# Kernel tuning notes

Hardware: AMD Instinct MI355X
Metric: run time of the kernel (lower is better)

## Reference

```python
import jax, jax.numpy as jnp
import numpy as np


def _fo_pool(f, z):
    # c_t = f_t * c_{t-1} + z_t, c_0 = 0, scanned over axis 1 (seq).
    # Associative combine: (a1,b1) * (a2,b2) = (a1*a2, a2*b1 + b2)
    def combine(left, right):
        a1, b1 = left
        a2, b2 = right
        return a1 * a2, a2 * b1 + b2
    _, c = jax.lax.associative_scan(combine, (f, z), axis=1)
    return c


def setup_inputs() -> dict:
    key = jax.random.key(0)
    ks = jax.random.split(key, 10)
    B, S, D_in, D_model, D_mlp, n_cls = 32, 2048, 512, 1024, 1024, 128
    s = 0.02
    return {
        "x":  jax.random.normal(ks[0], (B, S, D_in), dtype=jnp.float32),
        "W":  jax.random.normal(ks[1], (D_in, 3 * D_model), dtype=jnp.float32) * s,  # Linear, bias=False
        "V":  jax.random.normal(ks[2], (D_in, 3 * D_model), dtype=jnp.float32) * s,
        "Vb": jax.random.normal(ks[3], (3 * D_model,), dtype=jnp.float32) * s,
        "W0": jax.random.normal(ks[4], (D_model, D_mlp), dtype=jnp.float32) * s,
        "b0": jax.random.normal(ks[5], (D_mlp,), dtype=jnp.float32) * s,
        "W1": jax.random.normal(ks[6], (D_mlp, D_mlp), dtype=jnp.float32) * s,
        "b1": jax.random.normal(ks[7], (D_mlp,), dtype=jnp.float32) * s,
        "W2": jax.random.normal(ks[8], (D_mlp, n_cls), dtype=jnp.float32) * s,
        "b2": jax.random.normal(ks[9], (n_cls,), dtype=jnp.float32) * s,
    }


def reference(x, W, V, Vb, W0, b0, W1, b1, W2, b2):
    # kernel_size=2 pre: W(x) + V(x shifted right by one, zero-padded)
    xprev = jnp.pad(x[:, :-1, :], ((0, 0), (1, 0), (0, 0)))  # [B,S,D_in]
    pre = jnp.einsum('bsd,dk->bsk', x, W) + jnp.einsum('bsd,dk->bsk', xprev, V) + Vb
    f, z, o = jnp.split(pre, 3, axis=-1)
    f = jax.nn.sigmoid(f)
    z = (1.0 - f) * jnp.tanh(z)
    o = jax.nn.sigmoid(o)
    c = _fo_pool(f, z)          # [B,S,D_model]
    h = c * o
    q = h[:, -1, :]             # last timestep
    # dropout is identity at inference (training=False)
    q = jax.nn.relu(q @ W0 + b0)
    q = jax.nn.relu(q @ W1 + b1)
    return q @ W2 + b2
```

## Files before the change

### kernel.cpp

```cpp
#include <hip/hip_runtime.h>
#include <cstdint>
#include <cstddef>


typedef __attribute__((ext_vector_type(8))) short short8;
typedef __attribute__((ext_vector_type(4))) float f32x4;

#define ZERO_OFF_E 6291456u
#define XB_OFF_E   8388608u
#define U_LDS_BASE 8256

__device__ __forceinline__ unsigned short f2bf(float f) {
  unsigned int u = __float_as_uint(f);
  u += 0x7fffu + ((u >> 16) & 1u);
  return (unsigned short)(u >> 16);
}

__device__ __forceinline__ unsigned stage_addr(int r, int c) {
  return (unsigned)(r * 64 + (((c + r + (r >> 2)) & 3) << 4));
}

__device__ __forceinline__ float sigmoidf_fast(float x) {
  return 1.f / (1.f + __expf(-x));
}
__device__ __forceinline__ float tanhf_fast(float x) {
  float a = fabsf(x);
  float e = __expf(-2.f * a);
  float t = (1.f - e) / (1.f + e);
  return copysignf(t, x);
}

__global__ void prologue_kernel(const float* __restrict__ x, const float* __restrict__ W,
                                const float* __restrict__ V,
                                const float* __restrict__ b0, const float* __restrict__ b1,
                                const float* __restrict__ b2,
                                unsigned short* __restrict__ xb, unsigned short* __restrict__ U,
                                float* __restrict__ q0, float* __restrict__ q1,
                                float* __restrict__ out, uint4* __restrict__ zpg) {
  __shared__ float T[64 * 65];
  const int bx = blockIdx.x;
  if (bx < 8192) {
    int base = bx * 1024 + threadIdx.x;
#pragma unroll
    for (int i = 0; i < 4; ++i) {
      int gid = base + i * 256;
      float4 v = ((const float4*)x)[gid];
      ushort4 o;
      o.x = f2bf(v.x); o.y = f2bf(v.y); o.z = f2bf(v.z); o.w = f2bf(v.w);
      ((ushort4*)xb)[gid] = o;
    }
  } else if (bx < 8704) {
    const int u = bx - 8192;
    const int j0 = (u & 31) * 64;
    const int k0 = (u >> 5) * 64;
    const int jl = threadIdx.x & 63;
    const int q  = threadIdx.x >> 6;
    const float* src = (k0 < 512) ? (W + (size_t)k0 * 3072) : (V + (size_t)(k0 - 512) * 3072);
#pragma unroll 4
    for (int i = 0; i < 16; ++i) {
      int kl = q * 16 + i;
      T[kl * 65 + jl] = src[(size_t)kl * 3072 + j0 + jl];
    }
    __syncthreads();
    const int kl = threadIdx.x & 63;
#pragma unroll 4
    for (int i = 0; i < 16; ++i) {
      int jj = q * 16 + i;
      U[(size_t)(j0 + jj) * 1024 + k0 + kl] = f2bf(T[kl * 65 + jj]);
    }
  } else if (bx < 8832) {
    int gid = (bx - 8704) * 256 + threadIdx.x;
    q0[gid] = b0[gid & 1023];
    q1[gid] = b1[gid & 1023];
    if (gid < 4096) out[gid] = b2[gid & 127];
  } else {
    zpg[threadIdx.x] = make_uint4(0u, 0u, 0u, 0u);
  }
}

template <bool USE_BF>
__global__ __launch_bounds__(256, 3) void qrnn_main(
    const unsigned short* __restrict__ wsb, const float* __restrict__ xf,
    const float* __restrict__ Vb,
    float* __restrict__ Fagg, float* __restrict__ Zagg) {
  __shared__ __align__(16) char smem[36864];

  const int dt = blockIdx.x;
  const int cj = blockIdx.y;
  const int b  = blockIdx.z;
  const int tid = threadIdx.x;
  const int lane = tid & 63;
  const int wid  = tid >> 6;
  const int wm = wid >> 1, wn = wid & 1;
  const int s0 = cj * 128;
  const int l15 = lane & 15, lc = lane >> 4;

  f32x4 acc[4][4];
#pragma unroll
  for (int i = 0; i < 4; ++i)
#pragma unroll
    for (int j = 0; j < 4; ++j) acc[i][j] = f32x4{0.f, 0.f, 0.f, 0.f};

  unsigned voffA[2];
  size_t offAF[2]; int zAF[2];
#pragma unroll
  for (int p = 0; p < 2; ++p) {
    int cw = tid + p * 256;
    int r = cw >> 2, c = cw & 3;
    int sg = s0 - 1 + r;
    voffA[p] = (sg < 0) ? (ZERO_OFF_E + (unsigned)(c * 8))
                        : (XB_OFF_E + (unsigned)(b * 2048 + sg) * 512u + (unsigned)(c * 8));
    zAF[p] = (sg < 0);
    offAF[p] = ((size_t)(b * 2048 + (sg < 0 ? 0 : sg)) << 9) + c * 8;
  }
  unsigned voffA3 = XB_OFF_E + (unsigned)(b * 2048 + s0 + 127) * 512u + (unsigned)((tid & 3) * 8);
  size_t offAF3 = ((size_t)(b * 2048 + s0 + 127) << 9) + (tid & 3) * 8;

  unsigned voffU[4];
#pragma unroll
  for (int k = 0; k < 4; ++k) {
    int uw = tid + k * 256;
    int r = uw >> 2, c = uw & 3;
    int col = r & 127, half = r >> 7;
    int j = (col < 64) ? (dt * 64 + col) : (1024 + dt * 64 + (col - 64));
    voffU[k] = (unsigned)(j * 1024 + half * 512 + c * 8);
  }

  unsigned wA[2], wU[4];
#pragma unroll
  for (int p = 0; p < 2; ++p) {
    int cw = tid + p * 256;
    wA[p] = stage_addr(cw >> 2, cw & 3);
  }
  const unsigned wA3 = stage_addr(128, tid & 3);
#pragma unroll
  for (int k = 0; k < 4; ++k) {
    int uw = tid + k * 256;
    wU[k] = U_LDS_BASE + stage_addr(uw >> 2, uw & 3);
  }

  unsigned roA[2][4], roU[2][4];
#pragma unroll
  for (int h2 = 0; h2 < 2; ++h2) {
#pragma unroll
    for (int mt = 0; mt < 4; ++mt) {
      int rr = wm * 64 + l15 + mt * 16 + 1 - h2;
      roA[h2][mt] = stage_addr(rr, lc);
    }
#pragma unroll
    for (int nt = 0; nt < 4; ++nt) {
      int rrU = h2 * 128 + wn * 64 + l15 + nt * 16;
      roU[h2][nt] = U_LDS_BASE + stage_addr(rrU, lc);
    }
  }

  uint4 pA0, pA1, pA3, pU0, pU1, pU2, pU3;

  auto load_stage = [&](int s) {
    const unsigned short* cur = wsb + s * 32;
    if constexpr (USE_BF) {
      pA0 = *(const uint4*)(cur + voffA[0]);
      pA1 = *(const uint4*)(cur + voffA[1]);
      if (tid < 4) pA3 = *(const uint4*)(cur + voffA3);
    } else {
      const float* curf = xf + s * 32;
#pragma unroll
      for (int p = 0; p < 2; ++p) {
        uint4 v = make_uint4(0u, 0u, 0u, 0u);
        if (!zAF[p]) {
          float4 a0 = *(const float4*)(curf + offAF[p]);
          float4 a1 = *(const float4*)(curf + offAF[p] + 4);
          v.x = (unsigned)f2bf(a0.x) | ((unsigned)f2bf(a0.y) << 16);
          v.y = (unsigned)f2bf(a0.z) | ((unsigned)f2bf(a0.w) << 16);
          v.z = (unsigned)f2bf(a1.x) | ((unsigned)f2bf(a1.y) << 16);
          v.w = (unsigned)f2bf(a1.z) | ((unsigned)f2bf(a1.w) << 16);
        }
        if (p == 0) pA0 = v; else pA1 = v;
      }
      if (tid < 4) {
        float4 a0 = *(const float4*)(curf + offAF3);
        float4 a1 = *(const float4*)(curf + offAF3 + 4);
        pA3.x = (unsigned)f2bf(a0.x) | ((unsigned)f2bf(a0.y) << 16);
        pA3.y = (unsigned)f2bf(a0.z) | ((unsigned)f2bf(a0.w) << 16);
        pA3.z = (unsigned)f2bf(a1.x) | ((unsigned)f2bf(a1.y) << 16);
        pA3.w = (unsigned)f2bf(a1.z) | ((unsigned)f2bf(a1.w) << 16);
      }
    }
    pU0 = *(const uint4*)(cur + voffU[0]);
    pU1 = *(const uint4*)(cur + voffU[1]);
    pU2 = *(const uint4*)(cur + voffU[2]);
    pU3 = *(const uint4*)(cur + voffU[3]);
  };

  load_stage(0);

#pragma unroll 1
  for (int s = 0; s < 16; ++s) {
    __syncthreads();
    *(uint4*)(smem + wA[0]) = pA0;
    *(uint4*)(smem + wA[1]) = pA1;
    if (tid < 4) *(uint4*)(smem + wA3) = pA3;
    *(uint4*)(smem + wU[0]) = pU0;
    *(uint4*)(smem + wU[1]) = pU1;
    *(uint4*)(smem + wU[2]) = pU2;
    *(uint4*)(smem + wU[3]) = pU3;
    __syncthreads();
    if (s < 15) load_stage(s + 1);
#pragma unroll
    for (int h2 = 0; h2 < 2; ++h2) {
      short8 bfr[4];
#pragma unroll
      for (int nt = 0; nt < 4; ++nt)
        bfr[nt] = *(const short8*)(smem + roU[h2][nt]);
#pragma unroll
      for (int mt = 0; mt < 4; ++mt) {
        short8 afr = *(const short8*)(smem + roA[h2][mt]);
#pragma unroll
        for (int nt = 0; nt < 4; ++nt)
          acc[mt][nt] = __builtin_amdgcn_mfma_f32_16x16x32_bf16(afr, bfr[nt], acc[mt][nt], 0, 0, 0);
      }
    }
  }

  float* fA   = (float*)smem;
  float* tzA  = (float*)(smem + 17408);
  float* segF = (float*)(smem + 34816);
  float* segZ = (float*)(smem + 35840);

  const int d = tid & 63;
  float vb[4];
#pragma unroll
  for (int nt = 0; nt < 4; ++nt)
    vb[nt] = Vb[wn * 1024 + dt * 64 + nt * 16 + l15];

  float F_run = 1.f, Z_run = 0.f;

  for (int ph = 0; ph < 2; ++ph) {
    __syncthreads();
    if (wm == ph) {
      float* dst = (wn == 0) ? fA : tzA;
#pragma unroll
      for (int mt = 0; mt < 4; ++mt)
#pragma unroll
        for (int nt = 0; nt < 4; ++nt)
#pragma unroll
          for (int rg = 0; rg < 4; ++rg) {
            int t = mt * 16 + ((lane >> 4) << 2) + rg;
            int c = nt * 16 + l15;
            float v = acc[mt][nt][rg] + vb[nt];
            v = (wn == 0) ? sigmoidf_fast(v) : tanhf_fast(v);
            dst[t * 68 + c] = v;
          }
    }
    __syncthreads();
    {
      int seg = tid >> 6;
      float F = 1.f, Z = 0.f;
#pragma unroll 4
      for (int i = 0; i < 16; ++i) {
        int t = seg * 16 + i;
        float f  = fA[t * 68 + d];
        float tz = tzA[t * 68 + d];
        float z = (1.f - f) * tz;
        Z = f * Z + z;
        F *= f;
      }
      segF[seg * 64 + d] = F;
      segZ[seg * 64 + d] = Z;
    }
    __syncthreads();
    if (tid < 64) {
#pragma unroll
      for (int sgi = 0; sgi < 4; ++sgi) {
        float Fs = segF[sgi * 64 + tid], Zs = segZ[sgi * 64 + tid];
        Z_run = Fs * Z_run + Zs;
        F_run *= Fs;
      }
    }
  }
  if (tid < 64) {
    size_t o = (((size_t)b * 16 + cj) << 10) + dt * 64 + tid;
    Fagg[o] = F_run;
    Zagg[o] = Z_run;
  }
}

__global__ void head_kernel(const float* __restrict__ x, const float* __restrict__ W,
                            const float* __restrict__ V, const float* __restrict__ Vb,
                            const float* __restrict__ Fagg, const float* __restrict__ Zagg,
                            float* __restrict__ h) {
  __shared__ float red[4][64];
  const int dl = threadIdx.x & 63;
  const int w  = threadIdx.x >> 6;
  const int d = blockIdx.x * 64 + dl;
  const int b = blockIdx.y;

  const float* xl = x + ((size_t)b * 2048 + 2047) * 512;
  const float* xp = xl - 512;
  const float* Wc = W + 2048 + d;
  const float* Vc = V + 2048 + d;
  float po = 0.f;
  const int k0 = w * 128;
#pragma unroll 8
  for (int k = k0; k < k0 + 128; ++k) {
    po += xl[k] * Wc[(size_t)k * 3072];
    po += xp[k] * Vc[(size_t)k * 3072];
  }
  red[w][dl] = po;
  __syncthreads();
  if (w == 0) {
    po = red[0][dl] + red[1][dl] + red[2][dl] + red[3][dl] + Vb[2048 + d];
    float c = 0.f;
#pragma unroll
    for (int j = 0; j < 16; ++j) {
      size_t o = (((size_t)b * 16 + j) << 10) + d;
      c = Fagg[o] * c + Zagg[o];
    }
    h[((size_t)b << 10) + d] = c * sigmoidf_fast(po);
  }
}

__global__ void mlp_atomic_kernel(const float* __restrict__ in, const float* __restrict__ Wt,
                                  float* __restrict__ out, int K, int N, int relu_in) {
  __shared__ float red[4][64];
  const int nl = threadIdx.x & 63;
  const int w  = threadIdx.x >> 6;
  const int n = blockIdx.x * 64 + nl;
  const int b = blockIdx.y;
  const int k0 = blockIdx.z * (K >> 2) + w * (K >> 4);
  const float* row = in + (size_t)b * K;
  const float* Wc = Wt + n;
  float s = 0.f;
#pragma unroll 8
  for (int k = k0; k < k0 + (K >> 4); ++k) {
    float v = row[k];
    if (relu_in) v = fmaxf(v, 0.f);
    s += v * Wc[(size_t)k * N];
  }
  red[w][nl] = s;
  __syncthreads();
  if (w == 0) {
    s = red[0][nl] + red[1][nl] + red[2][nl] + red[3][nl];
    atomicAdd(&out[(size_t)b * N + n], s);
  }
}

extern "C" void kernel_launch(void* const* d_in, const int* in_sizes, int n_in,
                              void* d_out, int out_size, void* d_ws, size_t ws_size,
                              hipStream_t stream) {
  const float* x  = (const float*)d_in[0];
  const float* W  = (const float*)d_in[1];
  const float* V  = (const float*)d_in[2];
  const float* Vb = (const float*)d_in[3];
  const float* W0 = (const float*)d_in[4];
  const float* b0 = (const float*)d_in[5];
  const float* W1 = (const float*)d_in[6];
  const float* b1 = (const float*)d_in[7];
  const float* W2 = (const float*)d_in[8];
  const float* b2 = (const float*)d_in[9];

  char* ws = (char*)d_ws;
  unsigned short* U = (unsigned short*)(ws);
  float* Fagg = (float*)(ws + (size_t)4 * 1024 * 1024);
  float* Zagg = (float*)(ws + (size_t)6 * 1024 * 1024);
  float* h    = (float*)(ws + (size_t)8 * 1024 * 1024);
  float* q0   = (float*)(ws + (size_t)8 * 1024 * 1024 + 256 * 1024);
  float* q1   = (float*)(ws + (size_t)8 * 1024 * 1024 + 512 * 1024);
  uint4* zpg  = (uint4*)(ws + (size_t)12 * 1024 * 1024);
  unsigned short* xb = (unsigned short*)(ws + (size_t)16 * 1024 * 1024);

  const size_t need_bf = (size_t)16 * 1024 * 1024 + (size_t)67108864;
  int use_bf = (ws_size >= need_bf) ? 1 : 0;

  prologue_kernel<<<8833, 256, 0, stream>>>(x, W, V, b0, b1, b2, xb, U, q0, q1,
                                            (float*)d_out, zpg);
  if (use_bf)
    qrnn_main<true><<<dim3(16, 16, 32), 256, 0, stream>>>((const unsigned short*)ws, x,
                                                          Vb, Fagg, Zagg);
  else
    qrnn_main<false><<<dim3(16, 16, 32), 256, 0, stream>>>((const unsigned short*)ws, x,
                                                           Vb, Fagg, Zagg);
  head_kernel<<<dim3(16, 32), 256, 0, stream>>>(x, W, V, Vb, Fagg, Zagg, h);
  mlp_atomic_kernel<<<dim3(16, 32, 4), 256, 0, stream>>>(h, W0, q0, 1024, 1024, 0);
  mlp_atomic_kernel<<<dim3(16, 32, 4), 256, 0, stream>>>(q0, W1, q1, 1024, 1024, 1);
  mlp_atomic_kernel<<<dim3(2, 32, 4), 256, 0, stream>>>(q1, W2, (float*)d_out, 1024, 128, 1);
}
```

Baseline: 602.8 us.

## Add larger-tile 512-thread QRNN GEMM kernel with direct global-to-LDS loads

Adds a new main kernel that handles a 256-timestep by 128-channel tile (for both f and z) per 512-thread block, in place of the previous 128x64 tile per 256-thread block. Operands are loaded straight into LDS with global_load_lds through a 4-stage ring buffer, and MFMA sections are bracketed by priority changes. The aim is more data reuse per block, fewer launched blocks and better latency hiding. The trade-offs are 128KB of LDS per block, which limits occupancy, and more accumulator registers. The head kernel now takes a chunk count to match the new Fagg/Zagg layout.

```diff
diff --git a/kernel.cpp b/kernel.cpp
--- a/kernel.cpp
+++ b/kernel.cpp
@@ -28,6 +28,12 @@
   float e = __expf(-2.f * a);
   float t = (1.f - e) / (1.f + e);
   return copysignf(t, x);
+}
+
+__device__ __forceinline__ void gload_lds16(const void* g, const char* lds) {
+  __builtin_amdgcn_global_load_lds(
+      (const __attribute__((address_space(1))) void*)(uintptr_t)g,
+      (__attribute__((address_space(3))) void*)(uint32_t)(uintptr_t)lds, 16, 0, 0);
 }
 
 __global__ void prologue_kernel(const float* __restrict__ x, const float* __restrict__ W,
@@ -78,6 +84,172 @@
   }
 }
 
+__global__ __launch_bounds__(512, 2) void qrnn_main8(
+    const unsigned short* __restrict__ wsb, const float* __restrict__ Vb,
+    float* __restrict__ Fagg, float* __restrict__ Zagg) {
+  __shared__ __align__(16) char smem[131072];
+
+  const int dt = blockIdx.x;
+  const int cj = blockIdx.y;
+  const int b  = blockIdx.z;
+  const int tid = threadIdx.x;
+  const int lane = tid & 63;
+  const int wid  = tid >> 6;
+  const int wm = wid >> 2, wn = wid & 3;
+  const int l15 = lane & 15, lc = lane >> 4;
+  const int s0 = cj * 256;
+
+  f32x4 acc[8][4];
+#pragma unroll
+  for (int i = 0; i < 8; ++i)
+#pragma unroll
+    for (int j = 0; j < 4; ++j) acc[i][j] = f32x4{0.f, 0.f, 0.f, 0.f};
+
+  unsigned eAx[2], eAp[2], eB[2];
+#pragma unroll
+  for (int i = 0; i < 2; ++i) {
+    int row_g = wid * 32 + i * 16 + (lane >> 2);
+    int q = (lane & 3) ^ ((row_g >> 1) & 3);
+    int tx = s0 + row_g;
+    eAx[i] = XB_OFF_E + (unsigned)(b * 2048 + tx) * 512u + (unsigned)(q * 8);
+    int tp = s0 - 1 + row_g;
+    eAp[i] = (tp < 0) ? (ZERO_OFF_E + (unsigned)(q * 8))
+                      : (XB_OFF_E + (unsigned)(b * 2048 + tp) * 512u + (unsigned)(q * 8));
+    int jj = (row_g < 128) ? (dt * 128 + row_g) : (1024 + dt * 128 + (row_g - 128));
+    eB[i] = (unsigned)jj * 1024u + (unsigned)(q * 8);
+  }
+
+  const unsigned swz = (unsigned)((lc ^ ((l15 >> 1) & 3)) << 4);
+  const unsigned oA = (unsigned)((wm * 128 + l15) * 64) + swz;
+  const unsigned oB = 16384u + (unsigned)((wn * 64 + l15) * 64) + swz;
+
+  auto stage = [&](int kt) {
+    const unsigned sbase = (unsigned)((kt & 3) << 15);
+    const unsigned kaddB = (unsigned)(kt * 32);
+    const unsigned kaddA = (kt < 16) ? kaddB : (unsigned)((kt - 16) * 32);
+    const bool xp = (kt < 16);
+#pragma unroll
+    for (int i = 0; i < 2; ++i) {
+      unsigned da = (unsigned)__builtin_amdgcn_readfirstlane(
+          (int)(sbase + (unsigned)(wid * 2048 + i * 1024)));
+      const unsigned short* src = wsb + ((xp ? eAx[i] : eAp[i]) + kaddA);
+      gload_lds16(src, smem + da);
+    }
+#pragma unroll
+    for (int i = 0; i < 2; ++i) {
+      unsigned db = (unsigned)__builtin_amdgcn_readfirstlane(
+          (int)(sbase + 16384u + (unsigned)(wid * 2048 + i * 1024)));
+      const unsigned short* src = wsb + (eB[i] + kaddB);
+      gload_lds16(src, smem + db);
+    }
+  };
+
+  stage(0); stage(1); stage(2);
+  asm volatile("s_waitcnt vmcnt(8)" ::: "memory");
+  __builtin_amdgcn_s_barrier();
+  __builtin_amdgcn_sched_barrier(0);
+
+#pragma unroll 1
+  for (int kt = 0; kt < 32; ++kt) {
+    const char* buf = smem + ((kt & 3) << 15);
+    short8 bfr[4], afr[4];
+#pragma unroll
+    for (int nt = 0; nt < 4; ++nt) bfr[nt] = *(const short8*)(buf + oB + nt * 1024);
+#pragma unroll
+    for (int m = 0; m < 4; ++m) afr[m] = *(const short8*)(buf + oA + m * 1024);
+    if (kt < 29) stage(kt + 3);
+    __builtin_amdgcn_s_barrier();
+    __builtin_amdgcn_s_setprio(1);
+#pragma unroll
+    for (int m = 0; m < 4; ++m)
+#pragma unroll
+      for (int nt = 0; nt < 4; ++nt)
+        acc[m][nt] = __builtin_amdgcn_mfma_f32_16x16x32_bf16(afr[m], bfr[nt], acc[m][nt], 0, 0, 0);
+    __builtin_amdgcn_s_setprio(0);
+    __builtin_amdgcn_s_barrier();
+#pragma unroll
+    for (int m = 0; m < 4; ++m) afr[m] = *(const short8*)(buf + oA + (m + 4) * 1024);
+    __builtin_amdgcn_s_barrier();
+    __builtin_amdgcn_s_setprio(1);
+#pragma unroll
+    for (int m = 0; m < 4; ++m)
+#pragma unroll
+      for (int nt = 0; nt < 4; ++nt)
+        acc[m + 4][nt] =
+            __builtin_amdgcn_mfma_f32_16x16x32_bf16(afr[m], bfr[nt], acc[m + 4][nt], 0, 0, 0);
+    __builtin_amdgcn_s_setprio(0);
+    if (kt <= 28)      asm volatile("s_waitcnt vmcnt(8)" ::: "memory");
+    else if (kt == 29) asm volatile("s_waitcnt vmcnt(4)" ::: "memory");
+    else               asm volatile("s_waitcnt vmcnt(0)" ::: "memory");
+    __builtin_amdgcn_s_barrier();
+    __builtin_amdgcn_sched_barrier(0);
+  }
+
+  float* fA   = (float*)smem;
+  float* tzA  = (float*)(smem + 33792);
+  float* segF = (float*)(smem + 67584);
+  float* segZ = (float*)(smem + 69632);
+
+  float vb[4];
+#pragma unroll
+  for (int nt = 0; nt < 4; ++nt)
+    vb[nt] = Vb[(wn >> 1) * 1024 + dt * 128 + (wn & 1) * 64 + nt * 16 + l15];
+
+  const int d = tid & 127;
+  const int seg = tid >> 7;
+  float F_run = 1.f, Z_run = 0.f;
+
+  for (int ph = 0; ph < 4; ++ph) {
+    __syncthreads();
+    if (wm == (ph >> 1)) {
+      float* dst = (wn < 2) ? fA : tzA;
+#pragma unroll
+      for (int m = 0; m < 4; ++m) {
+        const int mt = (ph & 1) * 4 + m;
+#pragma unroll
+        for (int nt = 0; nt < 4; ++nt)
+#pragma unroll
+          for (int rg = 0; rg < 4; ++rg) {
+            int t = m * 16 + (lc << 2) + rg;
+            int c = (wn & 1) * 64 + nt * 16 + l15;
+            float v = acc[mt][nt][rg] + vb[nt];
+            v = (wn < 2) ? sigmoidf_fast(v) : tanhf_fast(v);
+            dst[t * 132 + c] = v;
+          }
+      }
+    }
+    __syncthreads();
+    {
+      float F = 1.f, Z = 0.f;
+#pragma unroll 4
+      for (int i = 0; i < 16; ++i) {
+        int t = seg * 16 + i;
+        float f  = fA[t * 132 + d];
+        float tz = tzA[t * 132 + d];
+        float z = (1.f - f) * tz;
+        Z = f * Z + z;
+        F *= f;
+      }
+      segF[seg * 128 + d] = F;
+      segZ[seg * 128 + d] = Z;
+    }
+    __syncthreads();
+    if (tid < 128) {
+#pragma unroll
+      for (int sgi = 0; sgi < 4; ++sgi) {
+        float Fs = segF[sgi * 128 + tid], Zs = segZ[sgi * 128 + tid];
+        Z_run = Fs * Z_run + Zs;
+        F_run *= Fs;
+      }
+    }
+  }
+  if (tid < 128) {
+    size_t o = (((size_t)b * 8 + cj) << 10) + dt * 128 + tid;
+    Fagg[o] = F_run;
+    Zagg[o] = Z_run;
+  }
+}
+
 template <bool USE_BF>
 __global__ __launch_bounds__(256, 3) void qrnn_main(
     const unsigned short* __restrict__ wsb, const float* __restrict__ xf,
@@ -288,7 +460,7 @@
 __global__ void head_kernel(const float* __restrict__ x, const float* __restrict__ W,
                             const float* __restrict__ V, const float* __restrict__ Vb,
                             const float* __restrict__ Fagg, const float* __restrict__ Zagg,
-                            float* __restrict__ h) {
+                            float* __restrict__ h, int nch) {
   __shared__ float red[4][64];
   const int dl = threadIdx.x & 63;
   const int w  = threadIdx.x >> 6;
@@ -311,9 +483,8 @@
   if (w == 0) {
     po = red[0][dl] + red[1][dl] + red[2][dl] + red[3][dl] + Vb[2048 + d];
     float c = 0.f;
-#pragma unroll
-    for (int j = 0; j < 16; ++j) {
-      size_t o = (((size_t)b * 16 + j) << 10) + d;
+    for (int j = 0; j < nch; ++j) {
+      size_t o = (((size_t)b * nch + j) << 10) + d;
       c = Fagg[o] * c + Zagg[o];
     }
     h[((size_t)b << 10) + d] = c * sigmoidf_fast(po);
@@ -374,13 +545,14 @@
 
   prologue_kernel<<<8833, 256, 0, stream>>>(x, W, V, b0, b1, b2, xb, U, q0, q1,
                                             (float*)d_out, zpg);
-  if (use_bf)
-    qrnn_main<true><<<dim3(16, 16, 32), 256, 0, stream>>>((const unsigned short*)ws, x,
-                                                          Vb, Fagg, Zagg);
-  else
+  if (use_bf) {
+    qrnn_main8<<<dim3(8, 8, 32), 512, 0, stream>>>((const unsigned short*)ws, Vb, Fagg, Zagg);
+    head_kernel<<<dim3(16, 32), 256, 0, stream>>>(x, W, V, Vb, Fagg, Zagg, h, 8);
+  } else {
     qrnn_main<false><<<dim3(16, 16, 32), 256, 0, stream>>>((const unsigned short*)ws, x,
                                                            Vb, Fagg, Zagg);
-  head_kernel<<<dim3(16, 32), 256, 0, stream>>>(x, W, V, Vb, Fagg, Zagg, h);
+    head_kernel<<<dim3(16, 32), 256, 0, stream>>>(x, W, V, Vb, Fagg, Zagg, h, 16);
+  }
   mlp_atomic_kernel<<<dim3(16, 32, 4), 256, 0, stream>>>(h, W0, q0, 1024, 1024, 0);
   mlp_atomic_kernel<<<dim3(16, 32, 4), 256, 0, stream>>>(q0, W1, q1, 1024, 1024, 1);
   mlp_atomic_kernel<<<dim3(2, 32, 4), 256, 0, stream>>>(q1, W2, (float*)d_out, 1024, 128, 1);
```

Measured after the change: 909.8 us. 1.51x slower.
